# Kernel optimization log

Hardware: AMD Instinct MI355X
Metric: run time of the kernel (lower is better)

## Reference

```python
import jax, jax.numpy as jnp
import numpy as np

H = 768
NH = 12
HD = H // NH  # 64


def setup_inputs() -> dict:
    key = jax.random.key(0)
    ks = jax.random.split(key, 8)
    B, S = 4, 2048
    sc = 1.0 / np.sqrt(H)
    return {
        "hidden_states": jax.random.normal(ks[0], (B, S, H), dtype=jnp.float32),
        "attention_mask": jnp.zeros((B, 1, 1, S), dtype=jnp.float32),
        "Wq": jax.random.normal(ks[1], (H, H), dtype=jnp.float32) * sc,
        "bq": jnp.zeros((H,), dtype=jnp.float32),
        "Wk": jax.random.normal(ks[2], (H, H), dtype=jnp.float32) * sc,
        "bk": jnp.zeros((H,), dtype=jnp.float32),
        "Wv": jax.random.normal(ks[3], (H, H), dtype=jnp.float32) * sc,
        "bv": jnp.zeros((H,), dtype=jnp.float32),
    }


def _split_heads(x):
    # [B,S,H] -> [B,NH,S,HD]
    B, S, _ = x.shape
    return x.reshape(B, S, NH, HD).transpose(0, 2, 1, 3)


def reference(hidden_states, attention_mask, Wq, bq, Wk, bk, Wv, bv):
    q = _split_heads(hidden_states @ Wq + bq)
    k = _split_heads(hidden_states @ Wk + bk)
    v = _split_heads(hidden_states @ Wv + bv)
    # scores: [B,NH,S,S]
    scores = jnp.einsum("bhqd,bhkd->bhqk", q, k) / np.sqrt(HD)
    scores = scores + attention_mask
    probs = jax.nn.softmax(scores, axis=-1)  # dropout is identity in eval
    ctx = jnp.einsum("bhqk,bhkd->bhqd", probs, v)
    B, _, S, _ = ctx.shape
    return ctx.transpose(0, 2, 1, 3).reshape(B, S, H)
```

## Files before the change

kernel.cpp:

```cpp
#include <hip/hip_runtime.h>
#include <stdint.h>

typedef short bf16x8 __attribute__((ext_vector_type(8)));
typedef float f32x4  __attribute__((ext_vector_type(4)));
typedef float f32x16 __attribute__((ext_vector_type(16)));
typedef unsigned short u16;

#define B_  4
#define S_  2048
#define H_  768
#define NH_ 12
#define HD_ 64
#define NPROJ_N (3*H_)

static __device__ __forceinline__ u16 f2bf(float f) {
    union { float f; unsigned int u; } x; x.f = f;
    return (u16)((x.u + 0x8000u) >> 16);
}
static __device__ __forceinline__ bf16x8 ld8(const u16* p) {
    return *(const bf16x8*)(const void*)p;
}
static __device__ __forceinline__ void st8(u16* p, bf16x8 v) {
    *(bf16x8*)(void*)p = v;
}
static __device__ __forceinline__ void async_ld16(const u16* g, const short* l) {
    __builtin_amdgcn_global_load_lds(
        (__attribute__((address_space(1))) void*)g,
        (__attribute__((address_space(3))) void*)l,
        16, 0, 0);
}
static __device__ __forceinline__ unsigned cvtpk(float a, float b) {
    unsigned r;
    asm("v_cvt_pk_bf16_f32 %0, %1, %2" : "=v"(r) : "v"(a), "v"(b));
    return r;
}
static __device__ __forceinline__ void pl32swap(unsigned& a, unsigned& b) {
    asm("v_permlane32_swap_b32 %0, %1" : "+v"(a), "+v"(b));
}
static __device__ __forceinline__ bf16x8 mk8(unsigned a, unsigned b, unsigned c, unsigned d) {
    union { unsigned u[4]; bf16x8 v; } x;
    x.u[0] = a; x.u[1] = b; x.u[2] = c; x.u[3] = d;
    return x.v;
}

__global__ __launch_bounds__(256) void prep_kernel(const float* __restrict__ in,
                                                   u16* __restrict__ out,
                                                   const float* __restrict__ wq,
                                                   const float* __restrict__ wk,
                                                   const float* __restrict__ wv,
                                                   u16* __restrict__ wt) {
    __shared__ float t[32][33];
    const int blk = blockIdx.x;
    const int tid = threadIdx.x;
    if (blk < 6144) {
        int i = (blk * 256 + tid) * 4;
        float4 v = *(const float4*)(in + i);
        ushort4 o;
        o.x = f2bf(v.x); o.y = f2bf(v.y); o.z = f2bf(v.z); o.w = f2bf(v.w);
        *(ushort4*)(out + i) = o;
    } else {
        const int idx  = blk - 6144;
        const int proj = idx / 576;
        const int rem  = idx % 576;
        const int bx = rem % 24, by = rem / 24;
        const float* w = (proj == 0) ? wq : (proj == 1) ? wk : wv;
        u16* o = wt + (size_t)proj * H_ * H_;
        const int tx = tid & 31, ty = tid >> 5;
        const int n0 = bx * 32, k0 = by * 32;
        #pragma unroll
        for (int i = 0; i < 4; i++)
            t[ty + i * 8][tx] = w[(size_t)(k0 + ty + i * 8) * H_ + n0 + tx];
        __syncthreads();
        #pragma unroll
        for (int i = 0; i < 4; i++)
            o[(size_t)(n0 + ty + i * 8) * H_ + k0 + tx] = f2bf(t[tx][ty + i * 8]);
    }
}

__global__ __launch_bounds__(256) void qkv_gemm(const u16* __restrict__ A,
                                                const u16* __restrict__ Wt,
                                                const float* __restrict__ bq,
                                                const float* __restrict__ bk,
                                                const float* __restrict__ bv,
                                                u16* __restrict__ qo,
                                                u16* __restrict__ ko,
                                                u16* __restrict__ vto) {
    __shared__ alignas(16) short SMEM[4][128 * 64];

    const int tid  = threadIdx.x;
    const int wave = tid >> 6;
    const int lane = tid & 63;
    const int quad = lane >> 4;
    const int l16  = lane & 15;
    const int wm   = wave & 1;
    const int wn   = wave >> 1;

    const int id  = blockIdx.x;
    const int xcd = id & 7;
    const int j   = id >> 3;
    const int mi  = j & 7;
    const int ni  = j >> 3;
    const int m0 = (xcd * 8 + mi) * 128;
    const int n0 = ni * 128;

    int stR[4], stC[4];
    #pragma unroll
    for (int jj = 0; jj < 4; jj++) {
        const int lc = wave * 256 + jj * 64 + lane;
        stR[jj] = lc >> 3;
        stC[jj] = ((lc & 7) ^ (stR[jj] & 7)) * 8;
    }
    const int fx0 = (quad ^ (l16 & 7)) * 8;
    const int fx1 = fx0 ^ 32;

    f32x4 acc[4][4];
    #pragma unroll
    for (int i = 0; i < 4; i++)
        #pragma unroll
        for (int jj = 0; jj < 4; jj++) acc[i][jj] = (f32x4)0.0f;

#define GSTAGE(kt_, buf_)                                                                     \
    do {                                                                                      \
        const int kk_ = (kt_) * 64;                                                           \
        _Pragma("unroll")                                                                     \
        for (int jj = 0; jj < 4; jj++) {                                                      \
            async_ld16(A  + (size_t)(m0 + stR[jj]) * H_ + kk_ + stC[jj],                      \
                       &SMEM[(buf_) * 2][(wave * 256 + jj * 64) * 8]);                        \
            async_ld16(Wt + (size_t)(n0 + stR[jj]) * H_ + kk_ + stC[jj],                      \
                       &SMEM[(buf_) * 2 + 1][(wave * 256 + jj * 64) * 8]);                    \
        }                                                                                     \
    } while (0)

    GSTAGE(0, 0);
    __syncthreads();

    for (int kt = 0; kt < 12; kt++) {
        const int cur = kt & 1;
        if (kt + 1 < 12) GSTAGE(kt + 1, cur ^ 1);
        const short* As = SMEM[cur * 2];
        const short* Bs = SMEM[cur * 2 + 1];
        #pragma unroll
        for (int ks = 0; ks < 2; ks++) {
            const int fx = ks ? fx1 : fx0;
            bf16x8 af[4], bfr[4];
            #pragma unroll
            for (int i = 0; i < 4; i++)
                af[i] = *(const bf16x8*)(const void*)&As[(wm * 64 + i * 16 + l16) * 64 + fx];
            #pragma unroll
            for (int jj = 0; jj < 4; jj++)
                bfr[jj] = *(const bf16x8*)(const void*)&Bs[(wn * 64 + jj * 16 + l16) * 64 + fx];
            #pragma unroll
            for (int i = 0; i < 4; i++)
                #pragma unroll
                for (int jj = 0; jj < 4; jj++)
                    acc[i][jj] = __builtin_amdgcn_mfma_f32_16x16x32_bf16(af[i], bfr[jj], acc[i][jj], 0, 0, 0);
        }
        __syncthreads();
    }
#undef GSTAGE

    const int proj  = n0 / H_;
    const int hbase = (n0 % H_) >> 6;
    const float* bias = (proj == 0) ? bq : (proj == 1) ? bk : bv;
    u16* Ct = (u16*)SMEM;

    #pragma unroll
    for (int nj = 0; nj < 4; nj++) {
        const int nl = wn * 64 + nj * 16 + l16;
        const float bv_ = bias[(n0 % H_) + nl];
        #pragma unroll
        for (int mi2 = 0; mi2 < 4; mi2++) {
            #pragma unroll
            for (int r = 0; r < 4; r++) {
                const int ml = wm * 64 + mi2 * 16 + quad * 4 + r;
                const u16 val = f2bf(acc[mi2][nj][r] + bv_);
                if (proj < 2)
                    Ct[ml * 128 + ((nl + (ml & 15) * 8) & 127)] = val;
                else
                    Ct[nl * 128 + ((ml + (nl & 15) * 8) & 127)] = val;
            }
        }
    }
    __syncthreads();

    if (proj < 2) {
        u16* dst0 = (proj == 0) ? qo : ko;
        const int c = tid & 7;
        #pragma unroll
        for (int jj = 0; jj < 8; jj++) {
            const int idx = jj * 32 + (tid >> 3);
            const int ml = idx >> 1, h2 = idx & 1;
            const int nbase = h2 * 64 + c * 8;
            bf16x8 v8 = *(const bf16x8*)(const void*)&Ct[ml * 128 + ((nbase + (ml & 15) * 8) & 127)];
            const int m = m0 + ml;
            const int b = m >> 11, s = m & 2047;
            st8(dst0 + ((size_t)(b * NH_ + hbase + h2) * S_ + s) * HD_ + c * 8, v8);
        }
    } else {
        const int b = m0 >> 11;
        #pragma unroll
        for (int jj = 0; jj < 8; jj++) {
            const int nl = (tid >> 3) + (jj & 3) * 32;
            const int c  = (tid & 7) + (jj >> 2) * 8;
            bf16x8 v8 = *(const bf16x8*)(const void*)&Ct[nl * 128 + ((c * 8 + (nl & 15) * 8) & 127)];
            const int h2 = nl >> 6, d = nl & 63;
            st8(vto + ((size_t)(b * NH_ + hbase + h2) * HD_ + d) * S_ + (m0 & 2047) + c * 8, v8);
        }
    }
}

__global__ __launch_bounds__(256, 3) void attn_kernel(const u16* __restrict__ q,
                                                      const u16* __restrict__ k,
                                                      const u16* __restrict__ vt,
                                                      const float* __restrict__ mask,
                                                      float* __restrict__ out) {
    __shared__ alignas(16) short Ks[2][64 * 64];
    __shared__ alignas(16) short Vs[2][64 * 64];
    __shared__ alignas(16) float Ms[S_];

    const int tid  = threadIdx.x;
    const int wave = tid >> 6;
    const int lane = tid & 63;
    const int l32  = lane & 31;
    const int h    = lane >> 5;

    const int bh = blockIdx.x;
    const int b  = bh / NH_;
    const int q0 = blockIdx.y * 128;
    const float C1 = 0.125f * 1.44269504f;

    {
        const float* mrow = mask + (size_t)b * S_;
        float4 a0 = *(const float4*)(mrow + tid * 8);
        float4 a1 = *(const float4*)(mrow + tid * 8 + 4);
        a0.x *= 1.44269504f; a0.y *= 1.44269504f; a0.z *= 1.44269504f; a0.w *= 1.44269504f;
        a1.x *= 1.44269504f; a1.y *= 1.44269504f; a1.z *= 1.44269504f; a1.w *= 1.44269504f;
        *(float4*)(Ms + tid * 8)     = a0;
        *(float4*)(Ms + tid * 8 + 4) = a1;
    }

    const u16* qrow = q + ((size_t)bh * S_ + q0 + wave * 32 + l32) * HD_;
    bf16x8 qf[4];
    #pragma unroll
    for (int i = 0; i < 4; i++) qf[i] = ld8(qrow + i * 16 + h * 8);

    const u16* kbase = k  + (size_t)bh * S_ * HD_;
    const u16* vbase = vt + (size_t)bh * HD_ * S_;

    const int sRow = tid >> 3;
    const int sCol = ((tid & 7) ^ (sRow & 7)) * 8;
    const int rx   = l32 & 7;

    float lsacc[4] = {0.f, 0.f, 0.f, 0.f};
    f32x16 oacc0 = (f32x16)0.0f;
    f32x16 oacc1 = (f32x16)0.0f;

#define STAGE(kt_, buf_)                                                                           \
    do {                                                                                           \
        async_ld16(kbase + (size_t)(kt_) * 4096 + sRow * 64 + sCol,          &Ks[buf_][tid * 8]);  \
        async_ld16(kbase + (size_t)(kt_) * 4096 + (sRow + 32) * 64 + sCol,   &Ks[buf_][2048 + tid * 8]); \
        async_ld16(vbase + (size_t)sRow * S_ + (kt_) * 64 + sCol,            &Vs[buf_][tid * 8]);  \
        async_ld16(vbase + (size_t)(sRow + 32) * S_ + (kt_) * 64 + sCol,     &Vs[buf_][2048 + tid * 8]); \
    } while (0)

    STAGE(0, 0);
    __syncthreads();

    for (int kt = 0; kt < S_ / 64; kt++) {
        const int cur = kt & 1;
        if (kt + 1 < S_ / 64) STAGE(kt + 1, cur ^ 1);
        const short* Kc = Ks[cur];
        const short* Vc = Vs[cur];

        f32x16 s0 = (f32x16)0.0f;
        f32x16 s1 = (f32x16)0.0f;
        __builtin_amdgcn_s_setprio(1);
        #pragma unroll
        for (int i = 0; i < 4; i++) {
            const int ch = ((h + 2 * i) ^ rx) * 8;
            bf16x8 kf0 = *(const bf16x8*)(const void*)&Kc[l32 * 64 + ch];
            bf16x8 kf1 = *(const bf16x8*)(const void*)&Kc[(l32 + 32) * 64 + ch];
            s0 = __builtin_amdgcn_mfma_f32_32x32x16_bf16(kf0, qf[i], s0, 0, 0, 0);
            s1 = __builtin_amdgcn_mfma_f32_32x32x16_bf16(kf1, qf[i], s1, 0, 0, 0);
        }
        __builtin_amdgcn_s_setprio(0);

        const float* mb = Ms + kt * 64;
        unsigned w0[8], w1[8];
        #pragma unroll
        for (int c = 0; c < 4; c++) {
            const f32x4 m0 = *(const f32x4*)(mb + c * 8 + h * 4);
            const f32x4 m1 = *(const f32x4*)(mb + 32 + c * 8 + h * 4);
            const float p00 = __builtin_amdgcn_exp2f(__builtin_fmaf(s0[4*c+0], C1, m0[0]));
            const float p01 = __builtin_amdgcn_exp2f(__builtin_fmaf(s0[4*c+1], C1, m0[1]));
            const float p02 = __builtin_amdgcn_exp2f(__builtin_fmaf(s0[4*c+2], C1, m0[2]));
            const float p03 = __builtin_amdgcn_exp2f(__builtin_fmaf(s0[4*c+3], C1, m0[3]));
            const float p10 = __builtin_amdgcn_exp2f(__builtin_fmaf(s1[4*c+0], C1, m1[0]));
            const float p11 = __builtin_amdgcn_exp2f(__builtin_fmaf(s1[4*c+1], C1, m1[1]));
            const float p12 = __builtin_amdgcn_exp2f(__builtin_fmaf(s1[4*c+2], C1, m1[2]));
            const float p13 = __builtin_amdgcn_exp2f(__builtin_fmaf(s1[4*c+3], C1, m1[3]));
            w0[2*c]   = cvtpk(p00, p01);
            w0[2*c+1] = cvtpk(p02, p03);
            w1[2*c]   = cvtpk(p10, p11);
            w1[2*c+1] = cvtpk(p12, p13);
            lsacc[c] += ((p00 + p01) + (p02 + p03)) + ((p10 + p11) + (p12 + p13));
        }

        bf16x8 pa[4];
        #pragma unroll
        for (int t = 0; t < 2; t++) {
            {
                unsigned a = w0[4*t+0], bb = w0[4*t+2];
                pl32swap(a, bb);
                unsigned c2 = w0[4*t+1], dd = w0[4*t+3];
                pl32swap(c2, dd);
                pa[t] = mk8(a, c2, bb, dd);
            }
            {
                unsigned a = w1[4*t+0], bb = w1[4*t+2];
                pl32swap(a, bb);
                unsigned c2 = w1[4*t+1], dd = w1[4*t+3];
                pl32swap(c2, dd);
                pa[2 + t] = mk8(a, c2, bb, dd);
            }
        }

        __builtin_amdgcn_s_setprio(1);
        #pragma unroll
        for (int t = 0; t < 4; t++) {
            const int ch = ((h + 2 * t) ^ rx) * 8;
            bf16x8 vf0 = *(const bf16x8*)(const void*)&Vc[l32 * 64 + ch];
            bf16x8 vf1 = *(const bf16x8*)(const void*)&Vc[(l32 + 32) * 64 + ch];
            oacc0 = __builtin_amdgcn_mfma_f32_32x32x16_bf16(pa[t], vf0, oacc0, 0, 0, 0);
            oacc1 = __builtin_amdgcn_mfma_f32_32x32x16_bf16(pa[t], vf1, oacc1, 0, 0, 0);
        }
        __builtin_amdgcn_s_setprio(0);
        __syncthreads();
    }
#undef STAGE

    float lsum = ((lsacc[0] + lsacc[1]) + (lsacc[2] + lsacc[3]));
    lsum += __shfl_xor(lsum, 32);
    const float linv_own = 1.0f / lsum;
    const int hh = bh % NH_;
    #pragma unroll
    for (int r = 0; r < 16; r++) {
        const int qq = (r & 3) + 8 * (r >> 2) + 4 * h;
        const float linv = __shfl(linv_own, qq);
        const int s = q0 + wave * 32 + qq;
        float* orow = out + ((size_t)b * S_ + s) * H_ + hh * 64 + l32;
        orow[0]  = oacc0[r] * linv;
        orow[32] = oacc1[r] * linv;
    }
}

extern "C" void kernel_launch(void* const* d_in, const int* in_sizes, int n_in,
                              void* d_out, int out_size, void* d_ws, size_t ws_size,
                              hipStream_t stream) {
    const float* hidden = (const float*)d_in[0];
    const float* amask  = (const float*)d_in[1];
    const float* Wq     = (const float*)d_in[2];
    const float* bq     = (const float*)d_in[3];
    const float* Wk     = (const float*)d_in[4];
    const float* bk     = (const float*)d_in[5];
    const float* Wv     = (const float*)d_in[6];
    const float* bv     = (const float*)d_in[7];
    float* out = (float*)d_out;

    char* ws = (char*)d_ws;
    const size_t sz_hidden = (size_t)B_ * S_ * H_ * 2;
    const size_t sz_wt     = (size_t)NPROJ_N * H_ * 2;
    const size_t sz_qkv    = (size_t)B_ * S_ * H_ * 2;

    u16* hid_bf = (u16*)(ws);
    u16* wt     = (u16*)(ws + sz_hidden);
    u16* qbuf   = (u16*)(ws + sz_hidden + sz_wt);
    u16* kbuf   = (u16*)(ws + sz_hidden + sz_wt + sz_qkv);
    u16* vtbuf  = (u16*)(ws + sz_hidden + sz_wt + 2 * sz_qkv);

    prep_kernel<<<dim3(6144 + 1728), dim3(256), 0, stream>>>(
        hidden, hid_bf, Wq, Wk, Wv, wt);
    qkv_gemm<<<dim3(1152), dim3(256), 0, stream>>>(
        hid_bf, wt, bq, bk, bv, qbuf, kbuf, vtbuf);
    attn_kernel<<<dim3(B_ * NH_, S_ / 128), dim3(256), 0, stream>>>(
        qbuf, kbuf, vtbuf, amask, out);
}
```

Measured before the change: 204.1 us.

## Compute softmax row sums via MFMA with ones and prescale mask in prep

The per-row softmax denominator is now accumulated with an extra MFMA that multiplies the bf16 probability tile by a ones vector, replacing the VALU adds and the cross-lane shuffle reduction. The log2e mask prescaling moves into the prep kernel, which writes a scaled-mask buffer. Attention then reads mask values from global memory (L2/L1) each tile instead of from an LDS copy. This trades VALU work and 8KB of LDS for one more MFMA per step and per-tile global loads. The row sums now come from the bf16-rounded probabilities, which slightly changes numerics.

```diff
diff --git a/kernel.cpp b/kernel.cpp
--- a/kernel.cpp
+++ b/kernel.cpp
@@ -48,7 +48,9 @@
                                                    const float* __restrict__ wq,
                                                    const float* __restrict__ wk,
                                                    const float* __restrict__ wv,
-                                                   u16* __restrict__ wt) {
+                                                   u16* __restrict__ wt,
+                                                   const float* __restrict__ amask,
+                                                   float* __restrict__ msc) {
     __shared__ float t[32][33];
     const int blk = blockIdx.x;
     const int tid = threadIdx.x;
@@ -58,7 +60,7 @@
         ushort4 o;
         o.x = f2bf(v.x); o.y = f2bf(v.y); o.z = f2bf(v.z); o.w = f2bf(v.w);
         *(ushort4*)(out + i) = o;
-    } else {
+    } else if (blk < 7872) {
         const int idx  = blk - 6144;
         const int proj = idx / 576;
         const int rem  = idx % 576;
@@ -74,6 +76,14 @@
         #pragma unroll
         for (int i = 0; i < 4; i++)
             o[(size_t)(n0 + ty + i * 8) * H_ + k0 + tx] = f2bf(t[tx][ty + i * 8]);
+    } else {
+        const int i = ((blk - 7872) * 256 + tid) * 8;
+        float4 a0 = *(const float4*)(amask + i);
+        float4 a1 = *(const float4*)(amask + i + 4);
+        a0.x *= 1.44269504f; a0.y *= 1.44269504f; a0.z *= 1.44269504f; a0.w *= 1.44269504f;
+        a1.x *= 1.44269504f; a1.y *= 1.44269504f; a1.z *= 1.44269504f; a1.w *= 1.44269504f;
+        *(float4*)(msc + i)     = a0;
+        *(float4*)(msc + i + 4) = a1;
     }
 }
 
@@ -212,11 +222,10 @@
 __global__ __launch_bounds__(256, 3) void attn_kernel(const u16* __restrict__ q,
                                                       const u16* __restrict__ k,
                                                       const u16* __restrict__ vt,
-                                                      const float* __restrict__ mask,
+                                                      const float* __restrict__ msc,
                                                       float* __restrict__ out) {
     __shared__ alignas(16) short Ks[2][64 * 64];
     __shared__ alignas(16) short Vs[2][64 * 64];
-    __shared__ alignas(16) float Ms[S_];
 
     const int tid  = threadIdx.x;
     const int wave = tid >> 6;
@@ -229,16 +238,6 @@
     const int q0 = blockIdx.y * 128;
     const float C1 = 0.125f * 1.44269504f;
 
-    {
-        const float* mrow = mask + (size_t)b * S_;
-        float4 a0 = *(const float4*)(mrow + tid * 8);
-        float4 a1 = *(const float4*)(mrow + tid * 8 + 4);
-        a0.x *= 1.44269504f; a0.y *= 1.44269504f; a0.z *= 1.44269504f; a0.w *= 1.44269504f;
-        a1.x *= 1.44269504f; a1.y *= 1.44269504f; a1.z *= 1.44269504f; a1.w *= 1.44269504f;
-        *(float4*)(Ms + tid * 8)     = a0;
-        *(float4*)(Ms + tid * 8 + 4) = a1;
-    }
-
     const u16* qrow = q + ((size_t)bh * S_ + q0 + wave * 32 + l32) * HD_;
     bf16x8 qf[4];
     #pragma unroll
@@ -246,12 +245,18 @@
 
     const u16* kbase = k  + (size_t)bh * S_ * HD_;
     const u16* vbase = vt + (size_t)bh * HD_ * S_;
+    const float* mrow = msc + (size_t)b * S_ + h * 4;
 
     const int sRow = tid >> 3;
     const int sCol = ((tid & 7) ^ (sRow & 7)) * 8;
     const int rx   = l32 & 7;
 
-    float lsacc[4] = {0.f, 0.f, 0.f, 0.f};
+    union { unsigned u[4]; bf16x8 v; } one_;
+    one_.u[0] = 0x3F803F80u; one_.u[1] = 0x3F803F80u;
+    one_.u[2] = 0x3F803F80u; one_.u[3] = 0x3F803F80u;
+    const bf16x8 ones = one_.v;
+
+    f32x16 lsacc = (f32x16)0.0f;
     f32x16 oacc0 = (f32x16)0.0f;
     f32x16 oacc1 = (f32x16)0.0f;
 
@@ -268,6 +273,15 @@
 
     for (int kt = 0; kt < S_ / 64; kt++) {
         const int cur = kt & 1;
+
+        const float* mb = mrow + kt * 64;
+        f32x4 mm0[4], mm1[4];
+        #pragma unroll
+        for (int c = 0; c < 4; c++) {
+            mm0[c] = *(const f32x4*)(mb + c * 8);
+            mm1[c] = *(const f32x4*)(mb + 32 + c * 8);
+        }
+
         if (kt + 1 < S_ / 64) STAGE(kt + 1, cur ^ 1);
         const short* Kc = Ks[cur];
         const short* Vc = Vs[cur];
@@ -285,25 +299,21 @@
         }
         __builtin_amdgcn_s_setprio(0);
 
-        const float* mb = Ms + kt * 64;
         unsigned w0[8], w1[8];
         #pragma unroll
         for (int c = 0; c < 4; c++) {
-            const f32x4 m0 = *(const f32x4*)(mb + c * 8 + h * 4);
-            const f32x4 m1 = *(const f32x4*)(mb + 32 + c * 8 + h * 4);
-            const float p00 = __builtin_amdgcn_exp2f(__builtin_fmaf(s0[4*c+0], C1, m0[0]));
-            const float p01 = __builtin_amdgcn_exp2f(__builtin_fmaf(s0[4*c+1], C1, m0[1]));
-            const float p02 = __builtin_amdgcn_exp2f(__builtin_fmaf(s0[4*c+2], C1, m0[2]));
-            const float p03 = __builtin_amdgcn_exp2f(__builtin_fmaf(s0[4*c+3], C1, m0[3]));
-            const float p10 = __builtin_amdgcn_exp2f(__builtin_fmaf(s1[4*c+0], C1, m1[0]));
-            const float p11 = __builtin_amdgcn_exp2f(__builtin_fmaf(s1[4*c+1], C1, m1[1]));
-            const float p12 = __builtin_amdgcn_exp2f(__builtin_fmaf(s1[4*c+2], C1, m1[2]));
-            const float p13 = __builtin_amdgcn_exp2f(__builtin_fmaf(s1[4*c+3], C1, m1[3]));
+            const float p00 = __builtin_amdgcn_exp2f(__builtin_fmaf(s0[4*c+0], C1, mm0[c][0]));
+            const float p01 = __builtin_amdgcn_exp2f(__builtin_fmaf(s0[4*c+1], C1, mm0[c][1]));
+            const float p02 = __builtin_amdgcn_exp2f(__builtin_fmaf(s0[4*c+2], C1, mm0[c][2]));
+            const float p03 = __builtin_amdgcn_exp2f(__builtin_fmaf(s0[4*c+3], C1, mm0[c][3]));
+            const float p10 = __builtin_amdgcn_exp2f(__builtin_fmaf(s1[4*c+0], C1, mm1[c][0]));
+            const float p11 = __builtin_amdgcn_exp2f(__builtin_fmaf(s1[4*c+1], C1, mm1[c][1]));
+            const float p12 = __builtin_amdgcn_exp2f(__builtin_fmaf(s1[4*c+2], C1, mm1[c][2]));
+            const float p13 = __builtin_amdgcn_exp2f(__builtin_fmaf(s1[4*c+3], C1, mm1[c][3]));
             w0[2*c]   = cvtpk(p00, p01);
             w0[2*c+1] = cvtpk(p02, p03);
             w1[2*c]   = cvtpk(p10, p11);
             w1[2*c+1] = cvtpk(p12, p13);
-            lsacc[c] += ((p00 + p01) + (p02 + p03)) + ((p10 + p11) + (p12 + p13));
         }
 
         bf16x8 pa[4];
@@ -333,20 +343,18 @@
             bf16x8 vf1 = *(const bf16x8*)(const void*)&Vc[(l32 + 32) * 64 + ch];
             oacc0 = __builtin_amdgcn_mfma_f32_32x32x16_bf16(pa[t], vf0, oacc0, 0, 0, 0);
             oacc1 = __builtin_amdgcn_mfma_f32_32x32x16_bf16(pa[t], vf1, oacc1, 0, 0, 0);
+            lsacc = __builtin_amdgcn_mfma_f32_32x32x16_bf16(pa[t], ones, lsacc, 0, 0, 0);
         }
         __builtin_amdgcn_s_setprio(0);
         __syncthreads();
     }
 #undef STAGE
 
-    float lsum = ((lsacc[0] + lsacc[1]) + (lsacc[2] + lsacc[3]));
-    lsum += __shfl_xor(lsum, 32);
-    const float linv_own = 1.0f / lsum;
     const int hh = bh % NH_;
     #pragma unroll
     for (int r = 0; r < 16; r++) {
         const int qq = (r & 3) + 8 * (r >> 2) + 4 * h;
-        const float linv = __shfl(linv_own, qq);
+        const float linv = 1.0f / lsacc[r];
         const int s = q0 + wave * 32 + qq;
         float* orow = out + ((size_t)b * S_ + s) * H_ + hh * 64 + l32;
         orow[0]  = oacc0[r] * linv;
@@ -377,11 +385,12 @@
     u16* qbuf   = (u16*)(ws + sz_hidden + sz_wt);
     u16* kbuf   = (u16*)(ws + sz_hidden + sz_wt + sz_qkv);
     u16* vtbuf  = (u16*)(ws + sz_hidden + sz_wt + 2 * sz_qkv);
-
-    prep_kernel<<<dim3(6144 + 1728), dim3(256), 0, stream>>>(
-        hidden, hid_bf, Wq, Wk, Wv, wt);
+    float* msc  = (float*)(ws + sz_hidden + sz_wt + 3 * sz_qkv);
+
+    prep_kernel<<<dim3(6144 + 1728 + 4), dim3(256), 0, stream>>>(
+        hidden, hid_bf, Wq, Wk, Wv, wt, amask, msc);
     qkv_gemm<<<dim3(1152), dim3(256), 0, stream>>>(
         hid_bf, wt, bq, bk, bv, qbuf, kbuf, vtbuf);
     attn_kernel<<<dim3(B_ * NH_, S_ / 128), dim3(256), 0, stream>>>(
-        qbuf, kbuf, vtbuf, amask, out);
-}
+        qbuf, kbuf, vtbuf, msc, out);
+}
```

Result: slower. 213.1 us (+4.4%).
